# Kernel optimization log

Hardware: AMD Instinct MI355X
Metric: run time of the kernel (lower is better)

The kernel has to match this reference:

```python
import jax, jax.numpy as jnp
import numpy as np

B, N, D, H, DD = 4, 256, 768, 12, 64
HD = D // H  # head_dim = 64
SCALE = float(np.sqrt(HD))


def _layernorm(x, g, b, eps=1e-5):
    mu = jnp.mean(x, axis=-1, keepdims=True)
    var = jnp.var(x, axis=-1, keepdims=True)
    return (x - mu) / jnp.sqrt(var + eps) * g + b


def setup_inputs() -> dict:
    key = jax.random.key(0)
    ks = jax.random.split(key, 20)
    def w(k, shape, fan_in):
        return (jax.random.normal(k, shape, jnp.float32) / np.sqrt(fan_in)).astype(jnp.float32)
    x = jax.random.normal(ks[0], (B, N, D), jnp.float32)
    dist = jax.random.normal(ks[1], (B, N, N, DD), jnp.float32)
    mask = jax.random.randint(ks[2], (B, N, N), 0, 2) > 0
    eye = jnp.eye(N, dtype=bool)[None]
    edge_mask = jnp.logical_or(mask, eye)  # guarantee no fully-masked row
    return {
        'x': x, 'distance_features': dist, 'edge_mask': edge_mask,
        'qkv_w': w(ks[3], (D, 3 * D), D), 'qkv_b': jnp.zeros((3 * D,), jnp.float32),
        'out_w': w(ks[4], (D, D), D), 'out_b': jnp.zeros((D,), jnp.float32),
        'rb_w1': w(ks[5], (DD, D), DD), 'rb_b1': jnp.zeros((D,), jnp.float32),
        'rb_w2': w(ks[6], (D, H), D), 'rb_b2': jnp.zeros((H,), jnp.float32),
        'gate_w1': w(ks[7], (D, D), D), 'gate_b1': jnp.zeros((D,), jnp.float32),
        'gate_w2': w(ks[8], (D, D), D), 'gate_b2': jnp.zeros((D,), jnp.float32),
        'ff_w1': w(ks[9], (D, 2 * D), D), 'ff_b1': jnp.zeros((2 * D,), jnp.float32),
        'ff_w2': w(ks[10], (2 * D, D), 2 * D), 'ff_b2': jnp.zeros((D,), jnp.float32),
        'ln1_g': jnp.ones((D,), jnp.float32), 'ln1_b': jnp.zeros((D,), jnp.float32),
        'ln2_g': jnp.ones((D,), jnp.float32), 'ln2_b': jnp.zeros((D,), jnp.float32),
    }


def reference(x, distance_features, edge_mask, qkv_w, qkv_b, out_w, out_b,
              rb_w1, rb_b1, rb_w2, rb_b2, gate_w1, gate_b1, gate_w2, gate_b2,
              ff_w1, ff_b1, ff_w2, ff_b2, ln1_g, ln1_b, ln2_g, ln2_b):
    residual = x
    xn = _layernorm(x, ln1_g, ln1_b)
    qkv = xn @ qkv_w + qkv_b
    q, k, v = jnp.split(qkv, 3, axis=-1)
    q = q.reshape(B, N, H, HD)
    k = k.reshape(B, N, H, HD)
    v = v.reshape(B, N, H, HD)
    logits = jnp.einsum('bihd,bjhd->bhij', q, k) / SCALE
    bias = jax.nn.silu(distance_features @ rb_w1 + rb_b1) @ rb_w2 + rb_b2  # [B,N,N,H]
    logits = logits + jnp.transpose(bias, (0, 3, 1, 2))
    neg = jnp.finfo(logits.dtype).min
    logits = jnp.where(edge_mask[:, None, :, :], logits, neg)
    attn = jax.nn.softmax(logits, axis=-1)
    context = jnp.einsum('bhij,bjhd->bihd', attn, v).reshape(B, N, D)
    gated = jax.nn.silu(xn @ gate_w1 + gate_b1) @ gate_w2 + gate_b2
    x2 = residual + (context * jax.nn.sigmoid(gated)) @ out_w + out_b
    y = _layernorm(x2, ln2_g, ln2_b)
    ff = jax.nn.gelu(y @ ff_w1 + ff_b1, approximate=False) @ ff_w2 + ff_b2
    return x2 + ff
```

## Files before the change

### kernel.cpp

```cpp
#include <hip/hip_runtime.h>
#include <hip/hip_bf16.h>
#include <cmath>

#define U16 unsigned short

typedef __bf16 bf16x8_t __attribute__((ext_vector_type(8)));
typedef float f32x4_t __attribute__((ext_vector_type(4)));

union Frag { uint4 u4; unsigned u[4]; bf16x8_t b8; U16 s[8]; };

__device__ __forceinline__ float b2f(U16 u) {
  union { unsigned int i; float f; } x; x.i = ((unsigned int)u) << 16; return x.f;
}
__device__ __forceinline__ U16 f2b(float f) {
  union { float f; unsigned int i; } x; x.f = f;
  unsigned int r = x.i + 0x7FFFu + ((x.i >> 16) & 1u);
  return (U16)(r >> 16);
}
__device__ __forceinline__ unsigned cvt_pk_bf16(float a, float b) {
  union { __hip_bfloat162 h2; unsigned u; } x;
  x.h2 = __float22bfloat162_rn(make_float2(a, b));
  return x.u;
}
__device__ __forceinline__ float fast_silu(float z) {
  return z * __builtin_amdgcn_rcpf(1.f + __expf(-z));
}
__device__ __forceinline__ void load_lds16(const U16* g, U16* l) {
  __builtin_amdgcn_global_load_lds((const __attribute__((address_space(1))) void*)g,
                                   (__attribute__((address_space(3))) void*)l, 16, 0, 0);
}

__device__ __forceinline__ void ln_row(int row, const float* __restrict__ X,
                                       const float* __restrict__ gam,
                                       const float* __restrict__ bet,
                                       U16* __restrict__ Y) {
  int tid = threadIdx.x, lane = tid & 63, wave = tid >> 6;
  __shared__ float p1[4], p2[4];
  float v[3];
#pragma unroll
  for (int j = 0; j < 3; ++j) v[j] = X[(size_t)row * 768 + tid + j * 256];
  float s1 = v[0] + v[1] + v[2];
  float s2 = v[0] * v[0] + v[1] * v[1] + v[2] * v[2];
#pragma unroll
  for (int m = 32; m > 0; m >>= 1) {
    s1 += __shfl_xor(s1, m);
    s2 += __shfl_xor(s2, m);
  }
  if (lane == 0) { p1[wave] = s1; p2[wave] = s2; }
  __syncthreads();
  float t1 = p1[0] + p1[1] + p1[2] + p1[3];
  float t2 = p2[0] + p2[1] + p2[2] + p2[3];
  float mean = t1 * (1.f / 768.f);
  float var = t2 * (1.f / 768.f) - mean * mean;
  float rstd = rsqrtf(var + 1e-5f);
#pragma unroll
  for (int j = 0; j < 3; ++j) {
    int c = tid + j * 256;
    Y[(size_t)row * 768 + c] = f2b((v[j] - mean) * rstd * gam[c] + bet[c]);
  }
}

__global__ __launch_bounds__(256) void prep_kernel(
    const float* __restrict__ qkv_w, const float* __restrict__ out_w,
    const float* __restrict__ g1w, const float* __restrict__ g2w,
    const float* __restrict__ ff1w, const float* __restrict__ ff2w,
    const float* __restrict__ rb1w, const float* __restrict__ rb2w,
    const float* __restrict__ qkv_b, const float* __restrict__ gate_b1,
    U16* __restrict__ qkv_wT, U16* __restrict__ out_wT, U16* __restrict__ g1wT,
    U16* __restrict__ g2wT, U16* __restrict__ ff1wT, U16* __restrict__ ff2wT,
    U16* __restrict__ rb1wT, U16* __restrict__ rb2wL, float* __restrict__ qg_bias,
    const float* __restrict__ x, const float* __restrict__ ln1_g,
    const float* __restrict__ ln1_b, U16* __restrict__ xn) {
  int bid = blockIdx.x;
  if (bid >= 5868) {
    ln_row(bid - 5868, x, ln1_g, ln1_b, xn);
    return;
  }
  if (bid >= 5856) {
    int idx = (bid - 5856) * 256 + threadIdx.x;
    qg_bias[idx] = (idx < 2304) ? qkv_b[idx] : gate_b1[idx - 2304];
    return;
  }
  if (bid >= 5808) {
    int idx = (bid - 5808) * 256 + threadIdx.x;
    int j = idx & 7, lane = (idx >> 3) & 63, pp = idx >> 9;
    int row = lane & 15, col = pp * 32 + ((lane >> 4) << 3) + j;
    rb2wL[idx] = (row < 12) ? f2b(rb2w[col * 12 + row]) : (U16)0;
    return;
  }
  const float* in; U16* out; int R, C, base;
  if (bid < 1728)      { in = qkv_w; out = qkv_wT; R = 768;  C = 2304; base = 0; }
  else if (bid < 2304) { in = out_w; out = out_wT; R = 768;  C = 768;  base = 1728; }
  else if (bid < 2880) { in = g1w;   out = g1wT;   R = 768;  C = 768;  base = 2304; }
  else if (bid < 3456) { in = g2w;   out = g2wT;   R = 768;  C = 768;  base = 2880; }
  else if (bid < 4608) { in = ff1w;  out = ff1wT;  R = 768;  C = 1536; base = 3456; }
  else if (bid < 5760) { in = ff2w;  out = ff2wT;  R = 1536; C = 768;  base = 4608; }
  else                 { in = rb1w;  out = rb1wT;  R = 64;   C = 768;  base = 5760; }
  int bx = bid - base, tilesx = C / 32;
  int c0 = (bx % tilesx) * 32, r0 = (bx / tilesx) * 32;
  __shared__ float tile[32][33];
  int tx = threadIdx.x & 31, ty = threadIdx.x >> 5;
#pragma unroll
  for (int yy = 0; yy < 4; ++yy)
    tile[ty + yy * 8][tx] = in[(size_t)(r0 + ty + yy * 8) * C + c0 + tx];
  __syncthreads();
#pragma unroll
  for (int yy = 0; yy < 4; ++yy)
    out[(size_t)(c0 + ty + yy * 8) * R + r0 + tx] = f2b(tile[tx][ty + yy * 8]);
}

template <int EPI, bool OUTF32>
__device__ __forceinline__ void gemm_core(U16* sA, U16* sB,
                                          const U16* __restrict__ A,
                                          const U16* __restrict__ BT,
                                          const float* __restrict__ bias,
                                          const float* __restrict__ other,
                                          void* __restrict__ Cout,
                                          float* __restrict__ Cout2,
                                          int N, int K, int bx, int by) {
  int tid = threadIdx.x;
  int lane = tid & 63, wave = tid >> 6;
  int m0 = by * 64, n0 = bx * 64;
  int wm = (wave >> 1) * 32, wn = (wave & 1) * 32;
  int lm = lane & 15, lq = lane >> 4;
  int srow = tid >> 2, scol = (tid & 3) * 8;
  const U16* ag = A + (size_t)(m0 + srow) * K + scol;
  const U16* bg = BT + (size_t)(n0 + srow) * K + scol;
  int nit = K >> 5;
  load_lds16(ag, sA + tid * 8);
  load_lds16(bg, sB + tid * 8);
  f32x4_t acc[2][2] = {};
  for (int i = 0; i < nit; ++i) {
    __syncthreads();
    int cb = (i & 1) * 2048, nb = ((i + 1) & 1) * 2048;
    if (i + 1 < nit) {
      load_lds16(ag + (i + 1) * 32, sA + nb + tid * 8);
      load_lds16(bg + (i + 1) * 32, sB + nb + tid * 8);
    }
    Frag af[2], bf[2];
#pragma unroll
    for (int mt = 0; mt < 2; ++mt)
      af[mt].u4 = *(const uint4*)&sA[cb + (wm + mt * 16 + lm) * 32 + lq * 8];
#pragma unroll
    for (int nt = 0; nt < 2; ++nt)
      bf[nt].u4 = *(const uint4*)&sB[cb + (wn + nt * 16 + lm) * 32 + lq * 8];
#pragma unroll
    for (int mt = 0; mt < 2; ++mt)
#pragma unroll
      for (int nt = 0; nt < 2; ++nt)
        acc[mt][nt] = __builtin_amdgcn_mfma_f32_16x16x32_bf16(af[mt].b8, bf[nt].b8,
                                                              acc[mt][nt], 0, 0, 0);
  }
#pragma unroll
  for (int nt = 0; nt < 2; ++nt) {
    int gc = n0 + wn + nt * 16 + lm;
    float bz = bias[gc];
#pragma unroll
    for (int mt = 0; mt < 2; ++mt) {
#pragma unroll
      for (int r = 0; r < 4; ++r) {
        int gr = m0 + wm + mt * 16 + lq * 4 + r;
        float z = acc[mt][nt][r] + bz;
        if (EPI == 5) {
          if (gc < 2304) Cout2[(size_t)gr * 2304 + gc] = z;
          else ((U16*)Cout)[(size_t)gr * 768 + gc - 2304] = f2b(fast_silu(z));
          continue;
        }
        size_t idx = (size_t)gr * N + gc;
        float o;
        if (EPI == 0) o = z;
        else if (EPI == 1) o = fast_silu(z);
        else if (EPI == 2) o = 0.5f * z * (1.f + erff(z * 0.70710678118f));
        else if (EPI == 3) o = other[idx] * __builtin_amdgcn_rcpf(1.f + __expf(-z));
        else o = z + other[idx];
        if (OUTF32) ((float*)Cout)[idx] = o;
        else ((U16*)Cout)[idx] = f2b(o);
      }
    }
  }
}

template <int EPI, bool OUTF32>
__global__ __launch_bounds__(256) void gemm_bt(const U16* __restrict__ A,
                                               const U16* __restrict__ BT,
                                               const float* __restrict__ bias,
                                               const float* __restrict__ other,
                                               void* __restrict__ Cout,
                                               int N, int K) {
  __shared__ __align__(16) U16 sA[2 * 2048];
  __shared__ __align__(16) U16 sB[2 * 2048];
  gemm_core<EPI, OUTF32>(sA, sB, A, BT, bias, other, Cout, nullptr, N, K,
                         blockIdx.x, blockIdx.y);
}

__device__ void rb_body(int bid, const float* __restrict__ dist,
                        const U16* __restrict__ w1T, const float* __restrict__ b1,
                        const U16* __restrict__ w2L, const float* __restrict__ b2,
                        float* __restrict__ biasOut) {
  int tid = threadIdx.x;
  int lane = tid & 63, wave = tid >> 6;
  int lm = lane & 15, lq = lane >> 4;
  int r0 = bid * 256;
  float hb = (lm < 12) ? b2[lm] : 0.f;
  Frag bd[4][2];
#pragma unroll
  for (int g = 0; g < 4; ++g) {
    const float* ap = dist + (size_t)(r0 + (wave * 4 + g) * 16 + lm) * 64 + lq * 8;
    float4 v0 = ((const float4*)ap)[0];
    float4 v1 = ((const float4*)ap)[1];
    float4 v2 = ((const float4*)(ap + 32))[0];
    float4 v3 = ((const float4*)(ap + 32))[1];
    bd[g][0].u[0] = cvt_pk_bf16(v0.x, v0.y); bd[g][0].u[1] = cvt_pk_bf16(v0.z, v0.w);
    bd[g][0].u[2] = cvt_pk_bf16(v1.x, v1.y); bd[g][0].u[3] = cvt_pk_bf16(v1.z, v1.w);
    bd[g][1].u[0] = cvt_pk_bf16(v2.x, v2.y); bd[g][1].u[1] = cvt_pk_bf16(v2.z, v2.w);
    bd[g][1].u[2] = cvt_pk_bf16(v3.x, v3.y); bd[g][1].u[3] = cvt_pk_bf16(v3.z, v3.w);
  }
  const U16* w1p0 = w1T + (size_t)(((lm >> 2) << 3) + (lm & 3)) * 64 + lq * 8;
  const U16* w1p1 = w1p0 + 256;
  const U16* w2p = w2L + lane * 8;
  const float* b1p = b1 + lq * 8;
  f32x4_t bacc[4] = {{hb, hb, hb, hb}, {hb, hb, hb, hb}, {hb, hb, hb, hb}, {hb, hb, hb, hb}};

  auto loadw = [&](int j, Frag& f00, Frag& f01, Frag& f10, Frag& f11, Frag& fwb,
                   float4& fb0, float4& fb1) {
    const U16* p0 = w1p0 + (size_t)j * 2048;
    const U16* p1 = w1p1 + (size_t)j * 2048;
    f00.u4 = *(const uint4*)p0;
    f01.u4 = *(const uint4*)(p0 + 32);
    f10.u4 = *(const uint4*)p1;
    f11.u4 = *(const uint4*)(p1 + 32);
    fwb.u4 = *(const uint4*)(w2p + (size_t)j * 512);
    fb0 = *(const float4*)(b1p + j * 32);
    fb1 = *(const float4*)(b1p + j * 32 + 4);
  };
  auto comp = [&](Frag& f00, Frag& f01, Frag& f10, Frag& f11, Frag& fwb,
                  float4 fb0, float4 fb1) {
    f32x4_t cz0 = {fb0.x, fb0.y, fb0.z, fb0.w};
    f32x4_t cz1 = {fb1.x, fb1.y, fb1.z, fb1.w};
#pragma unroll
    for (int g = 0; g < 4; ++g) {
      f32x4_t z0 = cz0, z1 = cz1;
      z0 = __builtin_amdgcn_mfma_f32_16x16x32_bf16(f00.b8, bd[g][0].b8, z0, 0, 0, 0);
      z0 = __builtin_amdgcn_mfma_f32_16x16x32_bf16(f01.b8, bd[g][1].b8, z0, 0, 0, 0);
      z1 = __builtin_amdgcn_mfma_f32_16x16x32_bf16(f10.b8, bd[g][0].b8, z1, 0, 0, 0);
      z1 = __builtin_amdgcn_mfma_f32_16x16x32_bf16(f11.b8, bd[g][1].b8, z1, 0, 0, 0);
      float s0 = fast_silu(z0[0]), s1 = fast_silu(z0[1]);
      float s2 = fast_silu(z0[2]), s3 = fast_silu(z0[3]);
      float t0 = fast_silu(z1[0]), t1 = fast_silu(z1[1]);
      float t2 = fast_silu(z1[2]), t3 = fast_silu(z1[3]);
      Frag af2;
      af2.u[0] = cvt_pk_bf16(s0, s1); af2.u[1] = cvt_pk_bf16(s2, s3);
      af2.u[2] = cvt_pk_bf16(t0, t1); af2.u[3] = cvt_pk_bf16(t2, t3);
      bacc[g] = __builtin_amdgcn_mfma_f32_16x16x32_bf16(af2.b8, fwb.b8, bacc[g], 0, 0, 0);
    }
  };

  Frag e00, e01, e10, e11, ewb, o00, o01, o10, o11, owb;
  float4 eb0, eb1, ob0, ob1;
  loadw(0, e00, e01, e10, e11, ewb, eb0, eb1);
  for (int pp = 0; pp < 24; pp += 2) {
    loadw(pp + 1, o00, o01, o10, o11, owb, ob0, ob1);
    comp(e00, e01, e10, e11, ewb, eb0, eb1);
    if (pp + 2 < 24) loadw(pp + 2, e00, e01, e10, e11, ewb, eb0, eb1);
    comp(o00, o01, o10, o11, owb, ob0, ob1);
  }
  if (lm < 12) {
#pragma unroll
    for (int g = 0; g < 4; ++g) {
#pragma unroll
      for (int r = 0; r < 4; ++r) {
        int gr = r0 + (wave * 4 + g) * 16 + lq * 4 + r;
        int b = gr >> 16, rem = gr & 65535, i = rem >> 8, j = rem & 255;
        biasOut[(((size_t)b * 12 + lm) * 256 + i) * 256 + j] = bacc[g][r];
      }
    }
  }
}

__global__ __launch_bounds__(256) void qkvrb_kernel(
    const U16* __restrict__ xn, const U16* __restrict__ qg_wT,
    const float* __restrict__ qg_b, float* __restrict__ qkvb, U16* __restrict__ g1,
    const float* __restrict__ dist, const U16* __restrict__ rb1wT,
    const float* __restrict__ rb_b1, const U16* __restrict__ rb2wL,
    const float* __restrict__ rb_b2, float* __restrict__ biasB) {
  __shared__ __align__(16) U16 sA[2 * 2048];
  __shared__ __align__(16) U16 sB[2 * 2048];
  int bid = blockIdx.x;
  if (bid < 768) {
    gemm_core<5, false>(sA, sB, xn, qg_wT, qg_b, nullptr, g1, qkvb, 3072, 768,
                        bid % 48, bid / 48);
  } else {
    rb_body(bid - 768, dist, rb1wT, rb_b1, rb2wL, rb_b2, biasB);
  }
}

__global__ __launch_bounds__(256) void attn_kernel(const float* __restrict__ qkv,
                                                   const float* __restrict__ biasB,
                                                   const int* __restrict__ mask,
                                                   float* __restrict__ ctx) {
  int tid = threadIdx.x, lane = tid & 63, w = tid >> 6;
  int bh = blockIdx.y, b = bh / 12, h = bh % 12;
  int i0 = blockIdx.x * 16;
  __shared__ U16 sK[64 * 258];
  __shared__ float sQ[16][66];
  __shared__ float sP[4][4][256];
  {
    int r = tid >> 4, c = (tid & 15) * 4;
    *(float4*)&sQ[r][c] =
        *(const float4*)&qkv[((size_t)(b * 256 + i0 + r)) * 2304 + h * 64 + c];
  }
  {
    const float* kr = qkv + ((size_t)(b * 256 + w * 64)) * 2304 + 768 + h * 64 + lane;
#pragma unroll 8
    for (int rr = 0; rr < 64; ++rr) {
      float kv = kr[(size_t)rr * 2304];
      sK[lane * 258 + w * 64 + rr] = (U16)cvt_pk_bf16(kv, kv);
    }
  }
  __syncthreads();
  int iw = i0 + w * 4;
  float lacc[4][4] = {};
#pragma unroll 4
  for (int d = 0; d < 64; ++d) {
    float k0 = b2f(sK[d * 258 + lane]);
    float k1 = b2f(sK[d * 258 + 64 + lane]);
    float k2 = b2f(sK[d * 258 + 128 + lane]);
    float k3 = b2f(sK[d * 258 + 192 + lane]);
#pragma unroll
    for (int qi = 0; qi < 4; ++qi) {
      float qv = sQ[w * 4 + qi][d];
      lacc[qi][0] += qv * k0;
      lacc[qi][1] += qv * k1;
      lacc[qi][2] += qv * k2;
      lacc[qi][3] += qv * k3;
    }
  }
#pragma unroll
  for (int qi = 0; qi < 4; ++qi) {
    int gi = iw + qi;
    const float* brow = biasB + (((size_t)b * 12 + h) * 256 + gi) * 256;
    const int* mrow = mask + ((size_t)b * 256 + gi) * 256;
    float lg[4];
#pragma unroll
    for (int jc = 0; jc < 4; ++jc) {
      float lv = lacc[qi][jc] * 0.125f + brow[jc * 64 + lane];
      lg[jc] = mrow[jc * 64 + lane] ? lv : -1e30f;
    }
    float mx = fmaxf(fmaxf(lg[0], lg[1]), fmaxf(lg[2], lg[3]));
#pragma unroll
    for (int m = 32; m > 0; m >>= 1) mx = fmaxf(mx, __shfl_xor(mx, m));
    float e[4], sum = 0.f;
#pragma unroll
    for (int jc = 0; jc < 4; ++jc) { e[jc] = __expf(lg[jc] - mx); sum += e[jc]; }
#pragma unroll
    for (int m = 32; m > 0; m >>= 1) sum += __shfl_xor(sum, m);
    float inv = __builtin_amdgcn_rcpf(sum);
#pragma unroll
    for (int jc = 0; jc < 4; ++jc) sP[w][qi][jc * 64 + lane] = e[jc] * inv;
  }
  float ca[4] = {0.f, 0.f, 0.f, 0.f};
  const float* vcol = qkv + (size_t)b * 256 * 2304 + 1536 + h * 64 + lane;
#pragma unroll 2
  for (int j4 = 0; j4 < 256; j4 += 4) {
    float4 p0 = *(const float4*)&sP[w][0][j4];
    float4 p1 = *(const float4*)&sP[w][1][j4];
    float4 p2 = *(const float4*)&sP[w][2][j4];
    float4 p3 = *(const float4*)&sP[w][3][j4];
    const float* pp0 = (const float*)&p0;
    const float* pp1 = (const float*)&p1;
    const float* pp2 = (const float*)&p2;
    const float* pp3 = (const float*)&p3;
#pragma unroll
    for (int jj = 0; jj < 4; ++jj) {
      float v = vcol[(size_t)(j4 + jj) * 2304];
      ca[0] += pp0[jj] * v;
      ca[1] += pp1[jj] * v;
      ca[2] += pp2[jj] * v;
      ca[3] += pp3[jj] * v;
    }
  }
#pragma unroll
  for (int qi = 0; qi < 4; ++qi)
    ctx[((size_t)(b * 256 + iw + qi)) * 768 + h * 64 + lane] = ca[qi];
}

__global__ __launch_bounds__(256) void ln_kernel(const float* __restrict__ X,
                                                 const float* __restrict__ gam,
                                                 const float* __restrict__ bet,
                                                 U16* __restrict__ Y) {
  ln_row(blockIdx.x, X, gam, bet, Y);
}

extern "C" void kernel_launch(void* const* d_in, const int* in_sizes, int n_in,
                              void* d_out, int out_size, void* d_ws, size_t ws_size,
                              hipStream_t stream) {
  const float* x       = (const float*)d_in[0];
  const float* dist    = (const float*)d_in[1];
  const int* mask      = (const int*)d_in[2];
  const float* qkv_w   = (const float*)d_in[3];
  const float* qkv_b   = (const float*)d_in[4];
  const float* out_w   = (const float*)d_in[5];
  const float* out_b   = (const float*)d_in[6];
  const float* rb_w1   = (const float*)d_in[7];
  const float* rb_b1   = (const float*)d_in[8];
  const float* rb_w2   = (const float*)d_in[9];
  const float* rb_b2   = (const float*)d_in[10];
  const float* gate_w1 = (const float*)d_in[11];
  const float* gate_b1 = (const float*)d_in[12];
  const float* gate_w2 = (const float*)d_in[13];
  const float* gate_b2 = (const float*)d_in[14];
  const float* ff_w1   = (const float*)d_in[15];
  const float* ff_b1   = (const float*)d_in[16];
  const float* ff_w2   = (const float*)d_in[17];
  const float* ff_b2   = (const float*)d_in[18];
  const float* ln1_g   = (const float*)d_in[19];
  const float* ln1_b   = (const float*)d_in[20];
  const float* ln2_g   = (const float*)d_in[21];
  const float* ln2_b   = (const float*)d_in[22];

  char* w = (char*)d_ws;
  auto alloc = [&](size_t bytes) {
    char* p = w;
    w += (bytes + 255) & ~(size_t)255;
    return p;
  };
  U16* xn      = (U16*)alloc(1024 * 768 * 2);
  float* qkvb  = (float*)alloc((size_t)1024 * 2304 * 4);
  U16* qg_wT   = (U16*)alloc((size_t)3072 * 768 * 2);
  U16* qkv_wT  = qg_wT;
  U16* g1wT    = qg_wT + (size_t)2304 * 768;
  float* qg_b  = (float*)alloc(3072 * 4);
  U16* out_wT  = (U16*)alloc(768 * 768 * 2);
  U16* g2wT    = (U16*)alloc(768 * 768 * 2);
  U16* ff1wT   = (U16*)alloc(1536 * 768 * 2);
  U16* ff2wT   = (U16*)alloc(768 * 1536 * 2);
  U16* rb1wT   = (U16*)alloc(768 * 64 * 2);
  U16* rb2wL   = (U16*)alloc(24 * 64 * 8 * 2);
  float* biasB = (float*)alloc((size_t)4 * 12 * 256 * 256 * 4);
  float* ctx   = (float*)alloc(1024 * 768 * 4);
  U16* g1      = (U16*)alloc(1024 * 768 * 2);
  U16* cg      = (U16*)alloc(1024 * 768 * 2);
  float* x2    = (float*)alloc(1024 * 768 * 4);
  U16* y       = (U16*)alloc(1024 * 768 * 2);
  U16* f1      = (U16*)alloc(1024 * 1536 * 2);
  (void)ws_size; (void)in_sizes; (void)n_in; (void)out_size;

  prep_kernel<<<6892, 256, 0, stream>>>(qkv_w, out_w, gate_w1, gate_w2, ff_w1, ff_w2,
                                        rb_w1, rb_w2, qkv_b, gate_b1,
                                        qkv_wT, out_wT, g1wT, g2wT, ff1wT, ff2wT,
                                        rb1wT, rb2wL, qg_b, x, ln1_g, ln1_b, xn);
  qkvrb_kernel<<<1792, 256, 0, stream>>>(xn, qg_wT, qg_b, qkvb, g1,
                                         dist, rb1wT, rb_b1, rb2wL, rb_b2, biasB);
  attn_kernel<<<dim3(16, 48), 256, 0, stream>>>(qkvb, biasB, mask, ctx);
  gemm_bt<3, false><<<dim3(12, 16), 256, 0, stream>>>(g1, g2wT, gate_b2, ctx, cg,
                                                      768, 768);
  gemm_bt<4, true><<<dim3(12, 16), 256, 0, stream>>>(cg, out_wT, out_b, x, x2,
                                                     768, 768);
  ln_kernel<<<1024, 256, 0, stream>>>(x2, ln2_g, ln2_b, y);
  gemm_bt<2, false><<<dim3(24, 16), 256, 0, stream>>>(y, ff1wT, ff_b1, nullptr, f1,
                                                      1536, 768);
  gemm_bt<4, true><<<dim3(12, 16), 256, 0, stream>>>(f1, ff2wT, ff_b2, x2, (float*)d_out,
                                                     768, 1536);
}
```

Measured before the change: 327.2 us.

## Run gate GEMM concurrently with attention and fuse gating into out-proj

The gate GEMM no longer depends on the attention context: it now writes sigmoid(gate) only, and its blocks share one launch with the attention blocks so the two run side by side. A new out-projection kernel multiplies ctx by the stored sigmoid while staging its A tile into shared memory, then applies the bias and adds the residual. This removes one launch and the serial dependency between attention and the gate GEMM. In exchange, the combined kernel reserves the larger attention shared-memory footprint for every block, and the A operand now goes through a register-to-LDS path that is not double-buffered.

```diff
diff --git a/kernel.cpp b/kernel.cpp
--- a/kernel.cpp
+++ b/kernel.cpp
@@ -169,9 +169,8 @@
         size_t idx = (size_t)gr * N + gc;
         float o;
         if (EPI == 0) o = z;
-        else if (EPI == 1) o = fast_silu(z);
         else if (EPI == 2) o = 0.5f * z * (1.f + erff(z * 0.70710678118f));
-        else if (EPI == 3) o = other[idx] * __builtin_amdgcn_rcpf(1.f + __expf(-z));
+        else if (EPI == 6) o = __builtin_amdgcn_rcpf(1.f + __expf(-z));
         else o = z + other[idx];
         if (OUTF32) ((float*)Cout)[idx] = o;
         else ((U16*)Cout)[idx] = f2b(o);
@@ -294,16 +293,17 @@
   }
 }
 
-__global__ __launch_bounds__(256) void attn_kernel(const float* __restrict__ qkv,
-                                                   const float* __restrict__ biasB,
-                                                   const int* __restrict__ mask,
-                                                   float* __restrict__ ctx) {
+__device__ void attn_body(unsigned char* smem, int bid,
+                          const float* __restrict__ qkv,
+                          const float* __restrict__ biasB,
+                          const int* __restrict__ mask,
+                          float* __restrict__ ctx) {
+  U16* sK = (U16*)smem;
+  float(*sQ)[66] = (float(*)[66])(smem + 33024);
+  float* sP = (float*)(smem + 33024 + 4224);
   int tid = threadIdx.x, lane = tid & 63, w = tid >> 6;
-  int bh = blockIdx.y, b = bh / 12, h = bh % 12;
-  int i0 = blockIdx.x * 16;
-  __shared__ U16 sK[64 * 258];
-  __shared__ float sQ[16][66];
-  __shared__ float sP[4][4][256];
+  int bh = bid >> 4, b = bh / 12, h = bh % 12;
+  int i0 = (bid & 15) * 16;
   {
     int r = tid >> 4, c = (tid & 15) * 4;
     *(float4*)&sQ[r][c] =
@@ -356,16 +356,16 @@
     for (int m = 32; m > 0; m >>= 1) sum += __shfl_xor(sum, m);
     float inv = __builtin_amdgcn_rcpf(sum);
 #pragma unroll
-    for (int jc = 0; jc < 4; ++jc) sP[w][qi][jc * 64 + lane] = e[jc] * inv;
+    for (int jc = 0; jc < 4; ++jc) sP[(w * 4 + qi) * 256 + jc * 64 + lane] = e[jc] * inv;
   }
   float ca[4] = {0.f, 0.f, 0.f, 0.f};
   const float* vcol = qkv + (size_t)b * 256 * 2304 + 1536 + h * 64 + lane;
 #pragma unroll 2
   for (int j4 = 0; j4 < 256; j4 += 4) {
-    float4 p0 = *(const float4*)&sP[w][0][j4];
-    float4 p1 = *(const float4*)&sP[w][1][j4];
-    float4 p2 = *(const float4*)&sP[w][2][j4];
-    float4 p3 = *(const float4*)&sP[w][3][j4];
+    float4 p0 = *(const float4*)&sP[(w * 4 + 0) * 256 + j4];
+    float4 p1 = *(const float4*)&sP[(w * 4 + 1) * 256 + j4];
+    float4 p2 = *(const float4*)&sP[(w * 4 + 2) * 256 + j4];
+    float4 p3 = *(const float4*)&sP[(w * 4 + 3) * 256 + j4];
     const float* pp0 = (const float*)&p0;
     const float* pp1 = (const float*)&p1;
     const float* pp2 = (const float*)&p2;
@@ -382,6 +382,90 @@
 #pragma unroll
   for (int qi = 0; qi < 4; ++qi)
     ctx[((size_t)(b * 256 + iw + qi)) * 768 + h * 64 + lane] = ca[qi];
+}
+
+__global__ __launch_bounds__(256) void attn_gate_kernel(
+    const float* __restrict__ qkv, const float* __restrict__ biasB,
+    const int* __restrict__ mask, float* __restrict__ ctx,
+    const U16* __restrict__ g1, const U16* __restrict__ g2wT,
+    const float* __restrict__ gate_b2, U16* __restrict__ sg) {
+  __shared__ __align__(16) unsigned char smem[53632];
+  int bid = blockIdx.x;
+  if (bid < 768) {
+    attn_body(smem, bid, qkv, biasB, mask, ctx);
+  } else {
+    int g = bid - 768;
+    gemm_core<6, false>((U16*)smem, (U16*)(smem + 8192), g1, g2wT, gate_b2, nullptr,
+                        sg, nullptr, 768, 768, g % 12, g / 12);
+  }
+}
+
+__global__ __launch_bounds__(256) void outp_kernel(const float* __restrict__ ctx,
+                                                   const U16* __restrict__ sg,
+                                                   const U16* __restrict__ out_wT,
+                                                   const float* __restrict__ out_b,
+                                                   const float* __restrict__ x,
+                                                   float* __restrict__ x2) {
+  __shared__ __align__(16) U16 sA[64 * 32];
+  __shared__ __align__(16) U16 sB[2 * 2048];
+  int tid = threadIdx.x;
+  int lane = tid & 63, wave = tid >> 6;
+  int m0 = blockIdx.y * 64, n0 = blockIdx.x * 64;
+  int wm = (wave >> 1) * 32, wn = (wave & 1) * 32;
+  int lm = lane & 15, lq = lane >> 4;
+  int srow = tid >> 2, scol = (tid & 3) * 8;
+  const float* cg0 = ctx + (size_t)(m0 + srow) * 768 + scol;
+  const U16* sg0 = sg + (size_t)(m0 + srow) * 768 + scol;
+  const U16* bg = out_wT + (size_t)(n0 + srow) * 768 + scol;
+  load_lds16(bg, sB + tid * 8);
+  float4 ca0 = *(const float4*)cg0;
+  float4 ca1 = *(const float4*)(cg0 + 4);
+  Frag sa; sa.u4 = *(const uint4*)sg0;
+  f32x4_t acc[2][2] = {};
+  for (int i = 0; i < 24; ++i) {
+    __syncthreads();
+    int cb = (i & 1) * 2048, nb = ((i + 1) & 1) * 2048;
+    if (i + 1 < 24) load_lds16(bg + (i + 1) * 32, sB + nb + tid * 8);
+    Frag av;
+    av.u[0] = cvt_pk_bf16(ca0.x * b2f(sa.s[0]), ca0.y * b2f(sa.s[1]));
+    av.u[1] = cvt_pk_bf16(ca0.z * b2f(sa.s[2]), ca0.w * b2f(sa.s[3]));
+    av.u[2] = cvt_pk_bf16(ca1.x * b2f(sa.s[4]), ca1.y * b2f(sa.s[5]));
+    av.u[3] = cvt_pk_bf16(ca1.z * b2f(sa.s[6]), ca1.w * b2f(sa.s[7]));
+    *(uint4*)&sA[tid * 8] = av.u4;
+    if (i + 1 < 24) {
+      ca0 = *(const float4*)(cg0 + (i + 1) * 32);
+      ca1 = *(const float4*)(cg0 + (i + 1) * 32 + 4);
+      sa.u4 = *(const uint4*)(sg0 + (i + 1) * 32);
+    }
+    __syncthreads();
+    Frag af[2], bf[2];
+#pragma unroll
+    for (int mt = 0; mt < 2; ++mt)
+      af[mt].u4 = *(const uint4*)&sA[(wm + mt * 16 + lm) * 32 + lq * 8];
+#pragma unroll
+    for (int nt = 0; nt < 2; ++nt)
+      bf[nt].u4 = *(const uint4*)&sB[cb + (wn + nt * 16 + lm) * 32 + lq * 8];
+#pragma unroll
+    for (int mt = 0; mt < 2; ++mt)
+#pragma unroll
+      for (int nt = 0; nt < 2; ++nt)
+        acc[mt][nt] = __builtin_amdgcn_mfma_f32_16x16x32_bf16(af[mt].b8, bf[nt].b8,
+                                                              acc[mt][nt], 0, 0, 0);
+  }
+#pragma unroll
+  for (int nt = 0; nt < 2; ++nt) {
+    int gc = n0 + wn + nt * 16 + lm;
+    float bz = out_b[gc];
+#pragma unroll
+    for (int mt = 0; mt < 2; ++mt) {
+#pragma unroll
+      for (int r = 0; r < 4; ++r) {
+        int gr = m0 + wm + mt * 16 + lq * 4 + r;
+        size_t idx = (size_t)gr * 768 + gc;
+        x2[idx] = acc[mt][nt][r] + bz + x[idx];
+      }
+    }
+  }
 }
 
 __global__ __launch_bounds__(256) void ln_kernel(const float* __restrict__ X,
@@ -439,7 +523,7 @@
   float* biasB = (float*)alloc((size_t)4 * 12 * 256 * 256 * 4);
   float* ctx   = (float*)alloc(1024 * 768 * 4);
   U16* g1      = (U16*)alloc(1024 * 768 * 2);
-  U16* cg      = (U16*)alloc(1024 * 768 * 2);
+  U16* sg      = (U16*)alloc(1024 * 768 * 2);
   float* x2    = (float*)alloc(1024 * 768 * 4);
   U16* y       = (U16*)alloc(1024 * 768 * 2);
   U16* f1      = (U16*)alloc(1024 * 1536 * 2);
@@ -451,11 +535,9 @@
                                         rb1wT, rb2wL, qg_b, x, ln1_g, ln1_b, xn);
   qkvrb_kernel<<<1792, 256, 0, stream>>>(xn, qg_wT, qg_b, qkvb, g1,
                                          dist, rb1wT, rb_b1, rb2wL, rb_b2, biasB);
-  attn_kernel<<<dim3(16, 48), 256, 0, stream>>>(qkvb, biasB, mask, ctx);
-  gemm_bt<3, false><<<dim3(12, 16), 256, 0, stream>>>(g1, g2wT, gate_b2, ctx, cg,
-                                                      768, 768);
-  gemm_bt<4, true><<<dim3(12, 16), 256, 0, stream>>>(cg, out_wT, out_b, x, x2,
-                                                     768, 768);
+  attn_gate_kernel<<<960, 256, 0, stream>>>(qkvb, biasB, mask, ctx,
+                                            g1, g2wT, gate_b2, sg);
+  outp_kernel<<<dim3(12, 16), 256, 0, stream>>>(ctx, sg, out_wT, out_b, x, x2);
   ln_kernel<<<1024, 256, 0, stream>>>(x2, ln2_g, ln2_b, y);
   gemm_bt<2, false><<<dim3(24, 16), 256, 0, stream>>>(y, ff1wT, ff_b1, nullptr, f1,
                                                       1536, 768);
```

New measurement: 326.2 us. Within noise of the previous version (-0.3%).
